# Kernel optimization log

Measured on AMD Instinct MI355X. Metric: run time of the kernel, lower is better.

## Reference

```python
import jax, jax.numpy as jnp
import numpy as np

N, E, D, H, FF = 50000, 800000, 128, 8, 512
DK = D // H
NTYPES = 5
EPS = 1e-5


def setup_inputs() -> dict:
    key = jax.random.key(0)
    ks = jax.random.split(key, 8)
    x = jax.random.normal(ks[0], (N, D), jnp.float32)
    edges = jax.random.randint(ks[1], (2, E), 0, N)
    etype = jax.random.randint(ks[2], (E,), 0, NTYPES)
    masks = etype[None, :] == jnp.arange(NTYPES)[:, None]  # [5, E] bool, exact partition
    s = 1.0 / np.sqrt(D)
    Wk = jax.random.normal(ks[3], (NTYPES, D, D), jnp.float32) * s
    bk = jnp.zeros((NTYPES, D), jnp.float32)
    ln1_g = jnp.ones((D,), jnp.float32)
    ln1_b = jnp.zeros((D,), jnp.float32)
    ln2_g = jnp.ones((D,), jnp.float32)
    ln2_b = jnp.zeros((D,), jnp.float32)
    W1 = jax.random.normal(ks[4], (D, FF), jnp.float32) * s
    b1 = jnp.zeros((FF,), jnp.float32)
    W2 = jax.random.normal(ks[5], (FF, D), jnp.float32) * (1.0 / np.sqrt(FF))
    b2 = jnp.zeros((D,), jnp.float32)
    return {"x": x, "edges": edges, "masks": masks, "Wk": Wk, "bk": bk,
            "ln1_g": ln1_g, "ln1_b": ln1_b, "ln2_g": ln2_g, "ln2_b": ln2_b,
            "W1": W1, "b1": b1, "W2": W2, "b2": b2}


def _layernorm(x, g, b):
    mu = x.mean(-1, keepdims=True)
    var = x.var(-1, keepdims=True)
    return (x - mu) * jax.lax.rsqrt(var + EPS) * g + b


def _proj(z, idx, masks, W, b):
    # per-edge-type masked linear: output[mask_i] = x[idx[mask_i]] @ W_i + b_i
    g = z[idx]  # [E, D] gather
    out = jnp.zeros((g.shape[0], D), z.dtype)
    for i in range(NTYPES):
        out = out + jnp.where(masks[i][:, None], g @ W[i] + b[i], 0.0)
    return out.reshape(-1, H, DK)  # [E, H, d_k]


def reference(x, edges, masks, Wk, bk, ln1_g, ln1_b, ln2_g, ln2_b, W1, b1, W2, b2):
    src, dst = edges[0], edges[1]
    n = x.shape[0]
    z = _layernorm(x, ln1_g, ln1_b)
    # source module uses self.key projection for query, key AND value
    q = _proj(z, src, masks, Wk, bk)   # [E, H, d_k]
    k = _proj(z, dst, masks, Wk, bk)   # [E, H, d_k]
    v = k                              # value = key(z, edges[1]) == key, reuse
    logits = (q * k).sum(2, keepdims=True)  # [E, H, 1], unscaled as in source
    m = jax.ops.segment_max(jax.lax.stop_gradient(logits), src, num_segments=n)
    scores = jnp.exp(logits - m[src])
    den = jax.ops.segment_sum(scores, src, num_segments=n)
    scores = scores / den[src]
    attn = jax.ops.segment_sum(scores * v, src, num_segments=n).reshape(n, -1)  # [N, D]
    x = x + attn
    z2 = _layernorm(x, ln2_g, ln2_b)
    ff = jax.nn.relu(z2 @ W1 + b1) @ W2 + b2
    return x + ff
```

## Files before the change

### kernel.cpp

```cpp
#include <hip/hip_runtime.h>

#define D 128
#define H 8
#define DK 16
#define FFDIM 512
#define NTYPES 5
#define LN_EPS 1e-5f

typedef __bf16 bf16x8 __attribute__((ext_vector_type(8)));
typedef float f32x4 __attribute__((ext_vector_type(4)));
typedef unsigned short ushort_t;
typedef unsigned int uint_t;

__device__ inline ushort_t bfbits(float f) {
  __bf16 b = (__bf16)f;
  return __builtin_bit_cast(ushort_t, b);
}

__global__ void detect_kernel(const unsigned char* __restrict__ m8, int E,
                              int* __restrict__ flag) {
  int lane = threadIdx.x;
  int s = 1;
  if (lane < E) {
    s = 0;
#pragma unroll
    for (int i = 0; i < NTYPES; ++i) s += (m8[(size_t)i * E + lane] != 0);
  }
  unsigned long long b = __ballot(s == 1);
  if (lane == 0) *flag = (b == ~0ull) ? 1 : 0;
}

__device__ inline int decode_etype(const unsigned char* __restrict__ m8,
                                   int E, int e, int is8) {
  int t = 0;
  if (is8) {
#pragma unroll
    for (int i = 1; i < NTYPES; ++i) t += i * (m8[(size_t)i * E + e] != 0);
  } else {
    const int* m32 = (const int*)m8;
#pragma unroll
    for (int i = 1; i < NTYPES; ++i) t += i * (m32[(size_t)i * E + e] != 0);
  }
  return t > (NTYPES - 1) ? (NTYPES - 1) : t;
}

__global__ void conv_frag_kernel(const float* __restrict__ W,
                                 ushort_t* __restrict__ hi,
                                 int K, int Ncol, size_t matW, size_t matF) {
  int gid = blockIdx.x * 256 + threadIdx.x;
  int total = (Ncol / 16) * (K / 32) * 64;
  if (gid >= total) return;
  const float* Wm = W + (size_t)blockIdx.y * matW;
  ushort_t* him = hi + (size_t)blockIdx.y * matF;
  int l = gid & 63;
  int ck = gid >> 6;
  int kk = ck % (K / 32);
  int c = ck / (K / 32);
  int row0 = kk * 32 + (l >> 4) * 8;
  int col = c * 16 + (l & 15);
  size_t ob = (size_t)gid * 8;
#pragma unroll
  for (int j = 0; j < 8; ++j) {
    float w = Wm[(size_t)(row0 + j) * Ncol + col];
    __bf16 h = (__bf16)w;
    him[ob + j] = __builtin_bit_cast(ushort_t, h);
  }
}

__global__ __launch_bounds__(256, 4) void projln_kernel(
    const float* __restrict__ x, const float* __restrict__ g,
    const float* __restrict__ b, const ushort_t* __restrict__ wkh,
    const float* __restrict__ bk, ushort_t* __restrict__ P, int n) {
  __shared__ ushort_t zsh[64 * D];
  __shared__ ushort_t zsl[64 * D];
  int tid = threadIdx.x, w = tid >> 6, l = tid & 63;
  int n0 = blockIdx.x * 64;

  for (int i = w; i < 64; i += 4) {
    int r = n0 + i;
    float v0 = 0.f, v1 = 0.f;
    if (r < n) {
      v0 = x[(size_t)r * D + l];
      v1 = x[(size_t)r * D + 64 + l];
    }
    float s = v0 + v1, ss = v0 * v0 + v1 * v1;
    for (int o = 32; o; o >>= 1) { s += __shfl_xor(s, o); ss += __shfl_xor(ss, o); }
    float mu = s * (1.f / D);
    float var = ss * (1.f / D) - mu * mu;
    float rs = rsqrtf(var + LN_EPS);
    float z0 = (v0 - mu) * rs * g[l] + b[l];
    float z1 = (v1 - mu) * rs * g[l + 64] + b[l + 64];
    int sw = (i & 7) << 3;
    int e0 = (i * D + l) ^ sw;
    int e1 = (i * D + l + 64) ^ sw;
    __bf16 h0 = (__bf16)z0, h1 = (__bf16)z1;
    zsh[e0] = __builtin_bit_cast(ushort_t, h0);
    zsh[e1] = __builtin_bit_cast(ushort_t, h1);
    __bf16 l0 = (__bf16)(z0 - (float)h0), l1 = (__bf16)(z1 - (float)h1);
    zsl[e0] = __builtin_bit_cast(ushort_t, l0);
    zsl[e1] = __builtin_bit_cast(ushort_t, l1);
  }
  __syncthreads();

  int lrow = w * 16 + (l & 15);
  int koff = (l >> 4) * 8;
  bf16x8 ah[4], al[4];
#pragma unroll
  for (int kk = 0; kk < 4; ++kk) {
    int e = (lrow * D + kk * 32 + koff) ^ ((lrow & 7) << 3);
    ah[kk] = *(const bf16x8*)(zsh + e);
    al[kk] = *(const bf16x8*)(zsl + e);
  }

  int col16 = l & 15, rgrp = (l >> 4) * 4;
  int rowbase = n0 + w * 16;
  for (int t = 0; t < NTYPES; ++t) {
    const ushort_t* bh0 = wkh + (size_t)t * (D * D);
    ushort_t* Pt = P + (size_t)t * n * D;
#pragma unroll
    for (int cp = 0; cp < 4; ++cp) {
      bf16x8 Bh[2][4];
#pragma unroll
      for (int cc = 0; cc < 2; ++cc)
#pragma unroll
        for (int kk = 0; kk < 4; ++kk) {
          size_t o = ((size_t)((cp * 2 + cc) * 4 + kk) * 64 + l) * 8;
          Bh[cc][kk] = *(const bf16x8*)(bh0 + o);
        }
      f32x4 aa[2], ac[2];
#pragma unroll
      for (int cc = 0; cc < 2; ++cc) {
        float bias = bk[t * D + (cp * 2 + cc) * 16 + col16];
        aa[cc] = (f32x4){bias, bias, bias, bias};
        ac[cc] = (f32x4){0.f, 0.f, 0.f, 0.f};
      }
#pragma unroll
      for (int kk = 0; kk < 4; ++kk)
#pragma unroll
        for (int cc = 0; cc < 2; ++cc) {
          aa[cc] = __builtin_amdgcn_mfma_f32_16x16x32_bf16(ah[kk], Bh[cc][kk], aa[cc], 0, 0, 0);
          ac[cc] = __builtin_amdgcn_mfma_f32_16x16x32_bf16(al[kk], Bh[cc][kk], ac[cc], 0, 0, 0);
        }
#pragma unroll
      for (int cc = 0; cc < 2; ++cc)
#pragma unroll
        for (int r = 0; r < 4; ++r) {
          int row = rowbase + rgrp + r;
          if (row < n)
            Pt[(size_t)row * D + (cp * 2 + cc) * 16 + col16] =
                bfbits(aa[cc][r] + ac[cc][r]);
        }
    }
  }
}

__global__ void zero_kernel(int* __restrict__ p, int n) {
  int i = blockIdx.x * 256 + threadIdx.x;
  if (i < n) p[i] = 0;
}

__global__ void hist5_kernel(const int* __restrict__ edges,
                             const unsigned char* __restrict__ masks,
                             const int* __restrict__ flag,
                             int* __restrict__ cnt5,
                             unsigned char* __restrict__ etype8, int E) {
  int e = blockIdx.x * 256 + threadIdx.x;
  if (e >= E) return;
  int t = decode_etype(masks, E, e, *flag);
  etype8[e] = (unsigned char)t;
  atomicAdd(&cnt5[edges[e] * 8 + t], 1);
}

__global__ __launch_bounds__(256) void scanA5_kernel(const int* __restrict__ cnt5,
                                                     int* __restrict__ loc,
                                                     int* __restrict__ bsums, int n) {
  __shared__ int ts[256];
  int tid = threadIdx.x;
  int i = blockIdx.x * 256 + tid;
  int v = 0;
  if (i < n) {
    int4 c0 = *(const int4*)(cnt5 + (size_t)i * 8);
    v = c0.x + c0.y + c0.z + c0.w + cnt5[(size_t)i * 8 + 4];
  }
  ts[tid] = v;
  __syncthreads();
  for (int o = 1; o < 256; o <<= 1) {
    int t = (tid >= o) ? ts[tid - o] : 0;
    __syncthreads();
    ts[tid] += t;
    __syncthreads();
  }
  if (i < n) loc[i] = ts[tid] - v;
  if (tid == 255) bsums[blockIdx.x] = ts[255];
}

__global__ __launch_bounds__(256) void scanB_kernel(int* __restrict__ bsums, int nb,
                                                    int* __restrict__ total) {
  __shared__ int ts[256];
  int tid = threadIdx.x;
  int per = (nb + 255) / 256;
  int start = tid * per;
  int end = min(start + per, nb);
  int s = 0;
  for (int i = start; i < end; ++i) s += bsums[i];
  ts[tid] = s;
  __syncthreads();
  for (int o = 1; o < 256; o <<= 1) {
    int t = (tid >= o) ? ts[tid - o] : 0;
    __syncthreads();
    ts[tid] += t;
    __syncthreads();
  }
  int run = ts[tid] - s;
  for (int i = start; i < end; ++i) {
    int v = bsums[i];
    bsums[i] = run;
    run += v;
  }
  if (tid == 255) *total = ts[255];
}

__global__ void build5_kernel(const int* __restrict__ loc,
                              const int* __restrict__ bsums,
                              const int* __restrict__ cnt5,
                              int* __restrict__ cursor5, int* __restrict__ tb,
                              int n) {
  int i = blockIdx.x * 256 + threadIdx.x;
  if (i >= n) return;
  int base = loc[i] + bsums[i >> 8];
#pragma unroll
  for (int t = 0; t < NTYPES; ++t) {
    int c = cnt5[(size_t)i * 8 + t];
    cursor5[(size_t)i * 8 + t] = base;
    tb[(size_t)i * 8 + t] = base;
    base += c;
  }
  tb[(size_t)i * 8 + 5] = base;
}

__global__ __launch_bounds__(256) void fill_kernel(
    const int* __restrict__ edges, const unsigned char* __restrict__ etype8,
    int* __restrict__ cursor5, int* __restrict__ elist, int E, int n) {
  int bx = blockIdx.x;
  int range = bx & 7;
  int e = (bx >> 3) * 256 + threadIdx.x;
  if (e >= E) return;
  int per = (n + 7) >> 3;
  int lo = range * per;
  int hi = min(lo + per, n);
  int src = edges[e];
  if (src < lo || src >= hi) return;
  int t = etype8[e];
  int dst = edges[E + e];
  int pos = atomicAdd(&cursor5[src * 8 + t], 1);
  elist[pos] = t * n + dst;
}

__global__ __launch_bounds__(256, 4) void attn_kernel(
    const float* __restrict__ x, const ushort_t* __restrict__ P,
    const int* __restrict__ tb, const int* __restrict__ elist,
    float* __restrict__ out, int n) {
  int node = (blockIdx.x * 256 + threadIdx.x) >> 4;
  int gl = threadIdx.x & 15;
  if (node >= n) return;

  int4 t03 = *(const int4*)(tb + (size_t)node * 8);
  int2 t45 = *(const int2*)(tb + (size_t)node * 8 + 4);
  int bnd0 = t03.x, bnd1 = t03.y, bnd2 = t03.z, bnd3 = t03.w;
  int bnd4 = t45.x, bnd5 = t45.y;

  float m = -1e30f, den = 0.f;
  float a[8];
#pragma unroll
  for (int i = 0; i < 8; ++i) a[i] = 0.f;

#pragma unroll
  for (int t = 0; t < NTYPES; ++t) {
    int jb = (t == 0) ? bnd0 : (t == 1) ? bnd1 : (t == 2) ? bnd2
             : (t == 3) ? bnd3 : bnd4;
    int je = (t == 0) ? bnd1 : (t == 1) ? bnd2 : (t == 2) ? bnd3
             : (t == 3) ? bnd4 : bnd5;
    if (jb >= je) continue;
    bf16x8 qb = *(const bf16x8*)(P + (size_t)(t * n + node) * D + gl * 8);
    float qf[8];
#pragma unroll
    for (int d = 0; d < 8; ++d) qf[d] = (float)qb[d];

    int row = elist[jb];
    bf16x8 kv = *(const bf16x8*)(P + (size_t)row * D + gl * 8);
    for (int j = jb; j < je; ++j) {
      bf16x8 kvn = kv;
      if (j + 1 < je) {
        int rn = elist[j + 1];
        kvn = *(const bf16x8*)(P + (size_t)rn * D + gl * 8);
      }
      float kf[8], p = 0.f;
#pragma unroll
      for (int d = 0; d < 8; ++d) {
        kf[d] = (float)kv[d];
        p += qf[d] * kf[d];
      }
      p += __shfl_xor(p, 1);
      float nm = fmaxf(m, p);
      float sc = __expf(m - nm);
      float w = __expf(p - nm);
      den = den * sc + w;
#pragma unroll
      for (int d = 0; d < 8; ++d) a[d] = a[d] * sc + w * kf[d];
      m = nm;
      kv = kvn;
    }
  }

  float inv = (bnd5 > bnd0) ? 1.f / den : 0.f;
  const float* xr = x + (size_t)node * D + gl * 8;
  float* orow = out + (size_t)node * D + gl * 8;
  float4 xa = *(const float4*)xr;
  float4 xb = *(const float4*)(xr + 4);
  float4 oa, ob;
  oa.x = xa.x + a[0] * inv; oa.y = xa.y + a[1] * inv;
  oa.z = xa.z + a[2] * inv; oa.w = xa.w + a[3] * inv;
  ob.x = xb.x + a[4] * inv; ob.y = xb.y + a[5] * inv;
  ob.z = xb.z + a[6] * inv; ob.w = xb.w + a[7] * inv;
  *(float4*)orow = oa;
  *(float4*)(orow + 4) = ob;
}

__global__ __launch_bounds__(256, 4) void ffn_mfma_kernel(
    const ushort_t* __restrict__ w1h, const ushort_t* __restrict__ w2h,
    const float* __restrict__ b1, const float* __restrict__ b2,
    const float* __restrict__ g, const float* __restrict__ bln,
    float* __restrict__ out, int n) {
  __shared__ ushort_t z2h[32 * D];
  __shared__ ushort_t z2l[32 * D];
  __shared__ float hb2[2][2][16 * 36];
  int tid = threadIdx.x, w = tid >> 6, l = tid & 63;
  int n0 = blockIdx.x * 32;
  int r2 = w >> 1, c2h = w & 1;

  for (int i = w; i < 32; i += 4) {
    int r = n0 + i;
    float v0 = 0.f, v1 = 0.f;
    if (r < n) {
      v0 = out[(size_t)r * D + l];
      v1 = out[(size_t)r * D + 64 + l];
    }
    float s = v0 + v1, ss = v0 * v0 + v1 * v1;
    for (int o = 32; o; o >>= 1) { s += __shfl_xor(s, o); ss += __shfl_xor(ss, o); }
    float mu = s * (1.f / D);
    float var = ss * (1.f / D) - mu * mu;
    float rs = rsqrtf(var + LN_EPS);
    float z0 = (v0 - mu) * rs * g[l] + bln[l];
    float z1 = (v1 - mu) * rs * g[l + 64] + bln[l + 64];
    int sw = (i & 7) << 3;
    int e0 = (i * D + l) ^ sw;
    int e1 = (i * D + l + 64) ^ sw;
    __bf16 h0 = (__bf16)z0, h1 = (__bf16)z1;
    z2h[e0] = __builtin_bit_cast(ushort_t, h0);
    z2h[e1] = __builtin_bit_cast(ushort_t, h1);
    __bf16 l0 = (__bf16)(z0 - (float)h0), l1 = (__bf16)(z1 - (float)h1);
    z2l[e0] = __builtin_bit_cast(ushort_t, l0);
    z2l[e1] = __builtin_bit_cast(ushort_t, l1);
  }
  __syncthreads();

  int lrow = r2 * 16 + (l & 15);
  int koff = (l >> 4) * 8;
  bf16x8 ah[4], al[4];
#pragma unroll
  for (int kk = 0; kk < 4; ++kk) {
    int e = (lrow * D + kk * 32 + koff) ^ ((lrow & 7) << 3);
    ah[kk] = *(const bf16x8*)(z2h + e);
    al[kk] = *(const bf16x8*)(z2l + e);
  }

  int col16 = l & 15, rgrp = (l >> 4) * 4;
  f32x4 acc2[4];
#pragma unroll
  for (int c = 0; c < 4; ++c) acc2[c] = (f32x4){0.f, 0.f, 0.f, 0.f};
  bf16x8 B2prev[4];

#pragma unroll
  for (int k = 0; k < 16; ++k) {
    int c = k * 2 + c2h;
    bf16x8 B1h[4], B2h[4];
#pragma unroll
    for (int kk = 0; kk < 4; ++kk) {
      size_t o = ((size_t)(c * 4 + kk) * 64 + l) * 8;
      B1h[kk] = *(const bf16x8*)(w1h + o);
    }
#pragma unroll
    for (int cc2 = 0; cc2 < 4; ++cc2) {
      int ct = c2h * 4 + cc2;
      size_t o = ((size_t)(ct * 16 + k) * 64 + l) * 8;
      B2h[cc2] = *(const bf16x8*)(w2h + o);
    }
    bf16x8 a2h, a2l;
    if (k > 0) {
      const float* hbr = &hb2[(k - 1) & 1][r2][0];
      float av[8];
      *(float4*)&av[0] = *(const float4*)&hbr[(l & 15) * 36 + koff];
      *(float4*)&av[4] = *(const float4*)&hbr[(l & 15) * 36 + koff + 4];
#pragma unroll
      for (int j = 0; j < 8; ++j) {
        __bf16 hv = (__bf16)av[j];
        a2h[j] = hv;
        a2l[j] = (__bf16)(av[j] - (float)hv);
      }
    }
    float bias = b1[c * 16 + col16];
    f32x4 ha = {bias, bias, bias, bias};
    f32x4 hc = {0.f, 0.f, 0.f, 0.f};
#pragma unroll
    for (int kk = 0; kk < 4; ++kk) {
      ha = __builtin_amdgcn_mfma_f32_16x16x32_bf16(ah[kk], B1h[kk], ha, 0, 0, 0);
      hc = __builtin_amdgcn_mfma_f32_16x16x32_bf16(al[kk], B1h[kk], hc, 0, 0, 0);
    }
    float* hbp = &hb2[k & 1][r2][0];
#pragma unroll
    for (int r = 0; r < 4; ++r)
      hbp[(rgrp + r) * 36 + c2h * 16 + col16] = fmaxf(ha[r] + hc[r], 0.f);
    if (k > 0) {
#pragma unroll
      for (int cc2 = 0; cc2 < 4; ++cc2) {
        acc2[cc2] = __builtin_amdgcn_mfma_f32_16x16x32_bf16(a2h, B2prev[cc2], acc2[cc2], 0, 0, 0);
        acc2[cc2] = __builtin_amdgcn_mfma_f32_16x16x32_bf16(a2l, B2prev[cc2], acc2[cc2], 0, 0, 0);
      }
    }
#pragma unroll
    for (int cc2 = 0; cc2 < 4; ++cc2) B2prev[cc2] = B2h[cc2];
    __syncthreads();
  }

  {
    const float* hbr = &hb2[1][r2][0];
    float av[8];
    *(float4*)&av[0] = *(const float4*)&hbr[(l & 15) * 36 + koff];
    *(float4*)&av[4] = *(const float4*)&hbr[(l & 15) * 36 + koff + 4];
    bf16x8 a2h, a2l;
#pragma unroll
    for (int j = 0; j < 8; ++j) {
      __bf16 hv = (__bf16)av[j];
      a2h[j] = hv;
      a2l[j] = (__bf16)(av[j] - (float)hv);
    }
#pragma unroll
    for (int cc2 = 0; cc2 < 4; ++cc2) {
      acc2[cc2] = __builtin_amdgcn_mfma_f32_16x16x32_bf16(a2h, B2prev[cc2], acc2[cc2], 0, 0, 0);
      acc2[cc2] = __builtin_amdgcn_mfma_f32_16x16x32_bf16(a2l, B2prev[cc2], acc2[cc2], 0, 0, 0);
    }
  }

#pragma unroll
  for (int cc2 = 0; cc2 < 4; ++cc2) {
    int col = (c2h * 4 + cc2) * 16 + col16;
    float bias2 = b2[col];
#pragma unroll
    for (int r = 0; r < 4; ++r) {
      int row = n0 + r2 * 16 + rgrp + r;
      if (row < n) {
        size_t o = (size_t)row * D + col;
        out[o] = out[o] + acc2[cc2][r] + bias2;
      }
    }
  }
}

extern "C" void kernel_launch(void* const* d_in, const int* in_sizes, int n_in,
                              void* d_out, int out_size, void* d_ws, size_t ws_size,
                              hipStream_t stream) {
  const float* x      = (const float*)d_in[0];
  const int* edges    = (const int*)d_in[1];
  const unsigned char* masks = (const unsigned char*)d_in[2];
  const float* Wk     = (const float*)d_in[3];
  const float* bk     = (const float*)d_in[4];
  const float* ln1_g  = (const float*)d_in[5];
  const float* ln1_b  = (const float*)d_in[6];
  const float* ln2_g  = (const float*)d_in[7];
  const float* ln2_b  = (const float*)d_in[8];
  const float* W1     = (const float*)d_in[9];
  const float* b1     = (const float*)d_in[10];
  const float* W2     = (const float*)d_in[11];
  const float* b2     = (const float*)d_in[12];
  float* out = (float*)d_out;

  const int n = in_sizes[0] / D;
  const int E = in_sizes[1] / 2;
  const int nbn = (n + 255) / 256;

  char* ws = (char*)d_ws;
  size_t off = 0;
  ushort_t* P = (ushort_t*)(ws + off);  off += (size_t)NTYPES * n * D * sizeof(ushort_t);
  int* cnt5   = (int*)(ws + off);       off += (size_t)n * 8 * sizeof(int);
  int* cursor5= (int*)(ws + off);       off += (size_t)n * 8 * sizeof(int);
  int* tb     = (int*)(ws + off);       off += (size_t)n * 8 * sizeof(int);
  int* loc    = (int*)(ws + off);       off += (size_t)n * sizeof(int);
  int* bsums  = (int*)(ws + off);       off += (size_t)nbn * sizeof(int);
  int* total  = (int*)(ws + off);       off += 64;
  int* elist  = (int*)(ws + off);       off += (size_t)E * sizeof(int);
  unsigned char* etype8 = (unsigned char*)(ws + off); off += (size_t)E + 64;
  int* flag   = (int*)(ws + off);       off += 64;
  ushort_t* wkh = (ushort_t*)(ws + off); off += (size_t)NTYPES * D * D * sizeof(ushort_t);
  ushort_t* w1h = (ushort_t*)(ws + off); off += (size_t)D * FFDIM * sizeof(ushort_t);
  ushort_t* w2h = (ushort_t*)(ws + off); off += (size_t)FFDIM * D * sizeof(ushort_t);
  (void)ws_size; (void)n_in; (void)out_size;

  detect_kernel<<<1, 64, 0, stream>>>(masks, E, flag);

  {
    dim3 gwk((8 * 4 * 64 + 255) / 256, NTYPES);
    conv_frag_kernel<<<gwk, 256, 0, stream>>>(Wk, wkh, D, D,
                                              (size_t)D * D, (size_t)D * D);
    dim3 gw1(((FFDIM / 16) * 4 * 64 + 255) / 256, 1);
    conv_frag_kernel<<<gw1, 256, 0, stream>>>(W1, w1h, D, FFDIM, 0, 0);
    dim3 gw2((8 * (FFDIM / 32) * 64 + 255) / 256, 1);
    conv_frag_kernel<<<gw2, 256, 0, stream>>>(W2, w2h, FFDIM, D, 0, 0);
  }

  projln_kernel<<<(n + 63) / 64, 256, 0, stream>>>(x, ln1_g, ln1_b, wkh, bk, P, n);

  zero_kernel<<<(n * 8 + 255) / 256, 256, 0, stream>>>(cnt5, n * 8);
  hist5_kernel<<<(E + 255) / 256, 256, 0, stream>>>(edges, masks, flag, cnt5, etype8, E);
  scanA5_kernel<<<nbn, 256, 0, stream>>>(cnt5, loc, bsums, n);
  scanB_kernel<<<1, 256, 0, stream>>>(bsums, nbn, total);
  build5_kernel<<<(n + 255) / 256, 256, 0, stream>>>(loc, bsums, cnt5, cursor5, tb, n);
  fill_kernel<<<((E + 255) / 256) * 8, 256, 0, stream>>>(edges, etype8, cursor5,
                                                         elist, E, n);

  attn_kernel<<<(n + 15) / 16, 256, 0, stream>>>(x, P, tb, elist, out, n);

  ffn_mfma_kernel<<<(n + 31) / 32, 256, 0, stream>>>(w1h, w2h,
                                                     b1, b2, ln2_g, ln2_b, out, n);
}
```

Before: 239.2 us.

## Split FFN hidden dimension across waves to remove per-step block barriers

The FFN kernel previously split output columns across wave pairs, which made the waves exchange hidden activations through shared memory with a __syncthreads on each of the 16 steps. Now each wave owns half of the hidden (FF) chunks for its 16 rows. It computes relu(z@W1) into a private shared buffer and accumulates the full 128-column W2 product itself. The two partial results are combined once at the end through a shared-memory reduction. This removes the per-iteration barriers but doubles the accumulator registers and drops the software prefetch of the W2 tiles.

```diff
diff --git a/kernel.cpp b/kernel.cpp
--- a/kernel.cpp
+++ b/kernel.cpp
@@ -331,12 +331,14 @@
     const float* __restrict__ b1, const float* __restrict__ b2,
     const float* __restrict__ g, const float* __restrict__ bln,
     float* __restrict__ out, int n) {
-  __shared__ ushort_t z2h[32 * D];
-  __shared__ ushort_t z2l[32 * D];
-  __shared__ float hb2[2][2][16 * 36];
+  __shared__ char smem[16640 + 4 * 2304];
+  ushort_t* z2h = (ushort_t*)smem;
+  ushort_t* z2l = (ushort_t*)(smem + 8192);
+  float* red = (float*)smem;
   int tid = threadIdx.x, w = tid >> 6, l = tid & 63;
   int n0 = blockIdx.x * 32;
-  int r2 = w >> 1, c2h = w & 1;
+  int r2 = w & 1, ph = w >> 1;
+  float* hbw = (float*)(smem + 16640) + w * 576;
 
   for (int i = w; i < 32; i += 4) {
     int r = n0 + i;
@@ -373,70 +375,45 @@
     ah[kk] = *(const bf16x8*)(z2h + e);
     al[kk] = *(const bf16x8*)(z2l + e);
   }
+  __syncthreads();
 
   int col16 = l & 15, rgrp = (l >> 4) * 4;
-  f32x4 acc2[4];
-#pragma unroll
-  for (int c = 0; c < 4; ++c) acc2[c] = (f32x4){0.f, 0.f, 0.f, 0.f};
-  bf16x8 B2prev[4];
-
-#pragma unroll
-  for (int k = 0; k < 16; ++k) {
-    int c = k * 2 + c2h;
-    bf16x8 B1h[4], B2h[4];
-#pragma unroll
-    for (int kk = 0; kk < 4; ++kk) {
-      size_t o = ((size_t)(c * 4 + kk) * 64 + l) * 8;
-      B1h[kk] = *(const bf16x8*)(w1h + o);
-    }
-#pragma unroll
-    for (int cc2 = 0; cc2 < 4; ++cc2) {
-      int ct = c2h * 4 + cc2;
-      size_t o = ((size_t)(ct * 16 + k) * 64 + l) * 8;
-      B2h[cc2] = *(const bf16x8*)(w2h + o);
-    }
-    bf16x8 a2h, a2l;
-    if (k > 0) {
-      const float* hbr = &hb2[(k - 1) & 1][r2][0];
-      float av[8];
-      *(float4*)&av[0] = *(const float4*)&hbr[(l & 15) * 36 + koff];
-      *(float4*)&av[4] = *(const float4*)&hbr[(l & 15) * 36 + koff + 4];
-#pragma unroll
-      for (int j = 0; j < 8; ++j) {
-        __bf16 hv = (__bf16)av[j];
-        a2h[j] = hv;
-        a2l[j] = (__bf16)(av[j] - (float)hv);
-      }
-    }
-    float bias = b1[c * 16 + col16];
-    f32x4 ha = {bias, bias, bias, bias};
-    f32x4 hc = {0.f, 0.f, 0.f, 0.f};
-#pragma unroll
-    for (int kk = 0; kk < 4; ++kk) {
-      ha = __builtin_amdgcn_mfma_f32_16x16x32_bf16(ah[kk], B1h[kk], ha, 0, 0, 0);
-      hc = __builtin_amdgcn_mfma_f32_16x16x32_bf16(al[kk], B1h[kk], hc, 0, 0, 0);
-    }
-    float* hbp = &hb2[k & 1][r2][0];
-#pragma unroll
-    for (int r = 0; r < 4; ++r)
-      hbp[(rgrp + r) * 36 + c2h * 16 + col16] = fmaxf(ha[r] + hc[r], 0.f);
-    if (k > 0) {
-#pragma unroll
-      for (int cc2 = 0; cc2 < 4; ++cc2) {
-        acc2[cc2] = __builtin_amdgcn_mfma_f32_16x16x32_bf16(a2h, B2prev[cc2], acc2[cc2], 0, 0, 0);
-        acc2[cc2] = __builtin_amdgcn_mfma_f32_16x16x32_bf16(a2l, B2prev[cc2], acc2[cc2], 0, 0, 0);
-      }
-    }
-#pragma unroll
-    for (int cc2 = 0; cc2 < 4; ++cc2) B2prev[cc2] = B2h[cc2];
-    __syncthreads();
-  }
-
-  {
-    const float* hbr = &hb2[1][r2][0];
+  f32x4 acc2[8];
+#pragma unroll
+  for (int c = 0; c < 8; ++c) acc2[c] = (f32x4){0.f, 0.f, 0.f, 0.f};
+
+  for (int i = 0; i < 8; ++i) {
+    int kk2 = 2 * i + ph;
+    bf16x8 B1h[2][4];
+#pragma unroll
+    for (int cc = 0; cc < 2; ++cc)
+#pragma unroll
+      for (int kk = 0; kk < 4; ++kk) {
+        size_t o = ((size_t)((kk2 * 2 + cc) * 4 + kk) * 64 + l) * 8;
+        B1h[cc][kk] = *(const bf16x8*)(w1h + o);
+      }
+    f32x4 ha[2], hc[2];
+#pragma unroll
+    for (int cc = 0; cc < 2; ++cc) {
+      float bias = b1[(kk2 * 2 + cc) * 16 + col16];
+      ha[cc] = (f32x4){bias, bias, bias, bias};
+      hc[cc] = (f32x4){0.f, 0.f, 0.f, 0.f};
+    }
+#pragma unroll
+    for (int kk = 0; kk < 4; ++kk)
+#pragma unroll
+      for (int cc = 0; cc < 2; ++cc) {
+        ha[cc] = __builtin_amdgcn_mfma_f32_16x16x32_bf16(ah[kk], B1h[cc][kk], ha[cc], 0, 0, 0);
+        hc[cc] = __builtin_amdgcn_mfma_f32_16x16x32_bf16(al[kk], B1h[cc][kk], hc[cc], 0, 0, 0);
+      }
+#pragma unroll
+    for (int cc = 0; cc < 2; ++cc)
+#pragma unroll
+      for (int r = 0; r < 4; ++r)
+        hbw[(rgrp + r) * 36 + cc * 16 + col16] = fmaxf(ha[cc][r] + hc[cc][r], 0.f);
     float av[8];
-    *(float4*)&av[0] = *(const float4*)&hbr[(l & 15) * 36 + koff];
-    *(float4*)&av[4] = *(const float4*)&hbr[(l & 15) * 36 + koff + 4];
+    *(float4*)&av[0] = *(const float4*)&hbw[(l & 15) * 36 + koff];
+    *(float4*)&av[4] = *(const float4*)&hbw[(l & 15) * 36 + koff + 4];
     bf16x8 a2h, a2l;
 #pragma unroll
     for (int j = 0; j < 8; ++j) {
@@ -445,22 +422,44 @@
       a2l[j] = (__bf16)(av[j] - (float)hv);
     }
 #pragma unroll
-    for (int cc2 = 0; cc2 < 4; ++cc2) {
-      acc2[cc2] = __builtin_amdgcn_mfma_f32_16x16x32_bf16(a2h, B2prev[cc2], acc2[cc2], 0, 0, 0);
-      acc2[cc2] = __builtin_amdgcn_mfma_f32_16x16x32_bf16(a2l, B2prev[cc2], acc2[cc2], 0, 0, 0);
-    }
-  }
-
-#pragma unroll
-  for (int cc2 = 0; cc2 < 4; ++cc2) {
-    int col = (c2h * 4 + cc2) * 16 + col16;
-    float bias2 = b2[col];
-#pragma unroll
-    for (int r = 0; r < 4; ++r) {
-      int row = n0 + r2 * 16 + rgrp + r;
-      if (row < n) {
-        size_t o = (size_t)row * D + col;
-        out[o] = out[o] + acc2[cc2][r] + bias2;
+    for (int half = 0; half < 2; ++half) {
+      bf16x8 B2h[4];
+#pragma unroll
+      for (int c2 = 0; c2 < 4; ++c2) {
+        int ct = half * 4 + c2;
+        size_t o = ((size_t)(ct * 16 + kk2) * 64 + l) * 8;
+        B2h[c2] = *(const bf16x8*)(w2h + o);
+      }
+#pragma unroll
+      for (int c2 = 0; c2 < 4; ++c2) {
+        int ct = half * 4 + c2;
+        acc2[ct] = __builtin_amdgcn_mfma_f32_16x16x32_bf16(a2h, B2h[c2], acc2[ct], 0, 0, 0);
+        acc2[ct] = __builtin_amdgcn_mfma_f32_16x16x32_bf16(a2l, B2h[c2], acc2[ct], 0, 0, 0);
+      }
+    }
+  }
+
+  if (ph == 0) {
+#pragma unroll
+    for (int ct = 0; ct < 8; ++ct)
+#pragma unroll
+      for (int r = 0; r < 4; ++r)
+        red[(r2 * 16 + rgrp + r) * 130 + ct * 16 + col16] = acc2[ct][r];
+  }
+  __syncthreads();
+  if (ph == 1) {
+#pragma unroll
+    for (int ct = 0; ct < 8; ++ct) {
+      int col = ct * 16 + col16;
+      float bias2 = b2[col];
+#pragma unroll
+      for (int r = 0; r < 4; ++r) {
+        int row = n0 + r2 * 16 + rgrp + r;
+        if (row < n) {
+          float part = red[(r2 * 16 + rgrp + r) * 130 + col];
+          size_t o = (size_t)row * D + col;
+          out[o] = out[o] + acc2[ct][r] + part + bias2;
+        }
       }
     }
   }
```

Measured after the change: 244.0 us. About the same (+2.0%).
